# Optimization experiments

Measured on AMD Instinct MI355X. Metric: run time of the kernel, lower is better.

## Reference

```python
import jax, jax.numpy as jnp
import numpy as np

# ---- model constants (match init_kwargs) ----
B, N, T, L = 16384, 32, 300, 1
DIM = 2                      # len(state_index)
DT = 1.0 / (T * L)           # dt = 1/(T*l)
STEPS = T * L                # Euler integration steps (time_steps = STEPS+1)
A_X = 1.0                    # canonical DMP phase constant
TAU = 1.0
HID = 64
OUT = N * DIM + DIM          # fc2_mean output size


def setup_inputs() -> dict:
    key = jax.random.key(0)
    ks = jax.random.split(key, 8)
    s = lambda i, shape, scale: jax.random.normal(ks[i], shape, jnp.float32) * scale
    inp = {
        "state": jax.random.normal(ks[0], (B, 3), jnp.float32),
        "fc1_w": s(1, (HID, 3), 0.3),
        "fc1_b": jnp.full((HID,), 0.1, jnp.float32),
        "fc2m_w": s(2, (OUT, HID), 0.1),
        "fc2m_b": jnp.full((OUT,), 0.1, jnp.float32),
        "sig_w": s(3, (DIM, HID), 0.1),
        "sig_b": jnp.zeros((DIM,), jnp.float32),
        "val_w": s(4, (DIM, HID), 0.1),
        "val_b": jnp.zeros((DIM,), jnp.float32),
    }
    # DMPParameters: gaussian RBF centers on exp-decayed phase, canonical widths
    c = jnp.exp(-A_X * jnp.linspace(0.0, 1.0, N))
    inp["dmp_c"] = c.astype(jnp.float32)
    inp["dmp_sigma2"] = (N ** 1.5 / c / A_X).astype(jnp.float32)
    return inp


def dmp_rollout(w, goal, y0, dy0, a_z, c, sigma2):
    """Euler rollout of DMP transformation system.
    w: [M,N] basis weights, goal/y0/dy0/a_z: [M] per-channel scalars.
    Returns Y, dY, ddY each [M, STEPS+1]."""
    z0 = dy0 * TAU
    b_z = a_z / 4.0

    def step(carry, _):
        x, y, z = carry
        x = x + (-A_X * x) * TAU * DT                       # phase update
        psi = jnp.exp(-0.5 * (x - c) ** 2 / sigma2)          # [N] gaussian RBF
        fx = (w @ psi) * x * (goal - y0) / jnp.sum(psi)      # [M] forcing term
        dz = a_z * (b_z * (goal - y) - z) + fx
        dy = z
        y = y + TAU * dy * DT
        z = z + TAU * dz * DT
        return (x, y, z), (y, dy * TAU, dz * TAU)

    _, (Ys, dYs, ddYs) = jax.lax.scan(
        step, (jnp.float32(1.0), y0, z0), None, length=STEPS)
    Y = jnp.concatenate([y0[None], Ys], axis=0).T            # [M, STEPS+1]
    dY = jnp.concatenate([dy0[None], dYs], axis=0).T
    ddY = jnp.concatenate([z0[None], ddYs], axis=0).T
    return Y, dY, ddY


def reference(state, fc1_w, fc1_b, fc2m_w, fc2m_b, sig_w, sig_b,
              val_w, val_b, dmp_c, dmp_sigma2):
    x = jnp.tanh(state @ fc1_w.T + fc1_b) * 0.1              # [B,64]
    y0 = state[:, :DIM].reshape(-1)                           # [M=B*DIM]
    dy0 = jnp.zeros_like(y0) + 0.01

    # value = fc2_value(x).repeat(1,T).view(-1,T,2).transpose(1,2) == broadcast over T
    v = x @ val_w.T + val_b                                   # [B,2]
    value = jnp.broadcast_to(v[:, :, None], (B, DIM, T))

    sigma = (jax.nn.sigmoid(x @ sig_w.T + sig_b) * 1.0 + 0.001).reshape(-1, DIM, 1)

    ndp_wg = x @ fc2m_w.T + fc2m_b                            # [B, 2N+2]
    goal = ndp_wg[:, :DIM].reshape(-1)                        # [M]
    w = ndp_wg[:, DIM:DIM * (N + 1)].reshape(-1, N)           # [M,N]
    a_z = jnp.clip(ndp_wg[:, -1], 0.5, 30.0)                  # learned a_z (az=True)
    a_z = jnp.broadcast_to(a_z[:, None], (B, DIM)).reshape(-1)

    Y, _, _ = dmp_rollout(w, goal, y0, dy0, a_z, dmp_c, dmp_sigma2)
    y = Y.reshape(B, DIM, -1)[:, :, ::L]                      # [B,2,T+1]
    a = y[:, :, 1:] - y[:, :, :-1]                            # [B,2,T]
    return (a, sigma, value)
```

## Files before the change

### kernel.cpp

```cpp
#include <hip/hip_runtime.h>
#include <hip/hip_bf16.h>

#define NB 32
#define TS 300
#define NBATCH 16384
#define DTF (1.0f/300.0f)
#define A_ELEMS (NBATCH*2*TS)

typedef __attribute__((ext_vector_type(8))) short bf16x8;
typedef __attribute__((ext_vector_type(4))) float f32x4;

static __device__ __forceinline__ ushort f2bf(float f) {
    union { __hip_bfloat16 h; ushort u; } cv;
    cv.h = __float2bfloat16(f);
    return cv.u;
}
static __device__ __forceinline__ float rdlane(float v, int lane) {
    return __int_as_float(__builtin_amdgcn_readlane(__float_as_int(v), lane));
}

__global__ __launch_bounds__(256) void k_fused(
    const float* __restrict__ state,
    const float* __restrict__ fc1_w, const float* __restrict__ fc1_b,
    const float* __restrict__ fc2m_w, const float* __restrict__ fc2m_b,
    const float* __restrict__ sig_w, const float* __restrict__ sig_b,
    const float* __restrict__ val_w, const float* __restrict__ val_b,
    const float* __restrict__ dmp_c, const float* __restrict__ dmp_s2,
    float* __restrict__ sig_out, float* __restrict__ a_out,
    float* __restrict__ v_out)
{
    __shared__ ushort phis[304*NB];
    __shared__ float  wlds[70*64];
    __shared__ float  f1[64*4];
    __shared__ ushort wloc[64*NB];
    __shared__ float4 ppl[64];
    __shared__ float4 xt[4][16][5];

    const int tid = threadIdx.x;
    const int wv  = tid >> 6;
    const int j   = tid & 63;

    for (int i = tid; i < 70*64; i += 256) {
        const int row = i >> 6, col = i & 63;
        float v;
        if (row < 66)      v = fc2m_w[i];
        else if (row < 68) v = sig_w[(row-66)*64 + col];
        else               v = val_w[(row-68)*64 + col];
        const int q = col >> 2, e = col & 3;
        wlds[row*64 + (((q ^ (row & 15)) << 2) | e)] = v;
    }
    if (tid < 64) {
        f1[tid*4+0] = fc1_w[tid*3+0];
        f1[tid*4+1] = fc1_w[tid*3+1];
        f1[tid*4+2] = fc1_w[tid*3+2];
        f1[tid*4+3] = fc1_b[tid];
    }
    {
        const float l2 = log2f(1.0f - DTF);
        for (int t = tid; t < 304; t += 256) {
            ushort row[NB];
            if (t < TS) {
                const float x = exp2f((float)(t + 1) * l2);
                float ps[NB]; float s = 0.0f;
                #pragma unroll
                for (int n = 0; n < NB; ++n) {
                    float d = x - dmp_c[n];
                    float p = __expf(-0.5f * d * d / dmp_s2[n]);
                    ps[n] = p; s += p;
                }
                const float inv = x / s;
                #pragma unroll
                for (int n = 0; n < NB; ++n) row[n] = f2bf(ps[n] * inv);
            } else {
                #pragma unroll
                for (int n = 0; n < NB; ++n) row[n] = 0;
            }
            uint4* dst = (uint4*)(phis + t*NB);
            #pragma unroll
            for (int q4 = 0; q4 < 4; ++q4) {
                union { ushort us[8]; uint4 v; } pk;
                #pragma unroll
                for (int e = 0; e < 8; ++e) pk.us[e] = row[q4*8 + e];
                dst[q4 ^ (t & 3)] = pk.v;
            }
        }
    }
    __syncthreads();

    {
        const int r2 = 64 + (j % 6);
        float wr[64], w2[64];
        #pragma unroll
        for (int q = 0; q < 16; ++q) {
            float4 a  = *(const float4*)(wlds + j*64  + ((q ^ (j  & 15)) << 2));
            wr[q*4+0]=a.x; wr[q*4+1]=a.y; wr[q*4+2]=a.z; wr[q*4+3]=a.w;
            float4 b4 = *(const float4*)(wlds + r2*64 + ((q ^ (r2 & 15)) << 2));
            w2[q*4+0]=b4.x; w2[q*4+1]=b4.y; w2[q*4+2]=b4.z; w2[q*4+3]=b4.w;
        }
        const float bias1 = fc2m_b[j];
        const float bias2 = (r2 < 66) ? fc2m_b[r2] : (r2 < 68) ? sig_b[r2-66] : val_b[r2-68];
        const float4 fw = *(const float4*)(f1 + j*4);

        const int bbase = (blockIdx.x << 5) + (wv << 3);
        float sreg = (j < 24) ? state[bbase*3 + j] : 0.0f;

        for (int it = 0; it < 8; ++it) {
            const float s0  = rdlane(sreg, it*3+0);
            const float s1  = rdlane(sreg, it*3+1);
            const float s2v = rdlane(sreg, it*3+2);
            float pre = fmaf(fw.x, s0, fmaf(fw.y, s1, fmaf(fw.z, s2v, fw.w)));
            float e = __expf(2.0f * pre);
            float h = (1.0f - 2.0f/(e + 1.0f)) * 0.1f;
            float a1 = bias1, a1b = 0.0f, a2 = bias2, a2b = 0.0f;
            #pragma unroll
            for (int k = 0; k < 64; k += 2) {
                const float h0 = rdlane(h, k);
                const float h1 = rdlane(h, k+1);
                a1  = fmaf(wr[k],   h0, a1 );
                a1b = fmaf(wr[k+1], h1, a1b);
                a2  = fmaf(w2[k],   h0, a2 );
                a2b = fmaf(w2[k+1], h1, a2b);
            }
            a1 += a1b; a2 += a2b;
            float az = rdlane(a2, 1);
            az = fminf(fmaxf(az, 0.5f), 30.0f);
            const float vv0 = rdlane(a2, 4);
            const float vv1 = rdlane(a2, 5);
            const int chp = (wv << 4) + (it << 1);
            if (j >= 2) wloc[(chp + ((j-2) >> 5))*NB + ((j-2) & 31)] = f2bf(a1);
            else        wloc[(chp + 1)*NB + 30 + j]                  = f2bf(a2);
            if (j == 2 || j == 3)
                sig_out[(bbase + it)*2 + j - 2] = 1.0f / (1.0f + __expf(-a2)) + 0.001f;
            if (j < 2) {
                const float y0 = (j == 0) ? s0 : s1;
                const float vvl = (j == 0) ? vv0 : vv1;
                ppl[chp + j] = make_float4(a1, a1 - y0, az, vvl);
            }
        }
    }
    __syncthreads();

    const int ch = j & 15;
    const int g  = j >> 4;
    const int chl = (wv << 4) + ch;

    const float4 pp = ppl[chl];
    const float az = pp.z;
    const float Ac = DTF * az * az * 0.25f;
    const float Bc = DTF * az;
    const float Kc = DTF * pp.y;
    const float c0 = Ac * pp.x;
    float y = pp.x - pp.y;
    float z = 0.01f;

    const bf16x8 wb = *(const bf16x8*)(wloc + chl*NB + g*8);
    const ushort* aprow = phis + ch*NB + ((g ^ (ch & 3)) << 3);
    bf16x8 af = *(const bf16x8*)aprow;

    const int mloc = j >> 2;
    const int m_st = (blockIdx.x << 6) + (wv << 4) + mloc;
    const float fv = ppl[(wv << 4) + mloc].w;
    const float4 vsp = make_float4(fv, fv, fv, fv);
    float* aptr = a_out + m_st*TS + (j & 3)*4;
    float* vptr = v_out + m_st*TS + (j & 3)*4;
    const bool tail_ok = (j & 3) < 3;

    const f32x4 zacc = {0.0f, 0.0f, 0.0f, 0.0f};

    for (int c = 0; c < 19; ++c) {
        f32x4 facc = __builtin_amdgcn_mfma_f32_16x16x32_bf16(af, wb, zacc, 0, 0, 0);
        if (c < 18) af = *(const bf16x8*)(aprow + (c + 1)*16*NB);

        float F[16];
        #pragma unroll
        for (int q = 0; q < 4; ++q) {
            float a = facc[q], b = facc[q];
            asm volatile("v_permlane16_swap_b32 %0, %1" : "+v"(a), "+v"(b));
            float a2 = a, b2 = b;
            asm volatile("v_permlane32_swap_b32 %0, %1" : "+v"(a), "+v"(a2));
            asm volatile("v_permlane32_swap_b32 %0, %1" : "+v"(b), "+v"(b2));
            F[0*4+q] = a; F[1*4+q] = b; F[2*4+q] = a2; F[3*4+q] = b2;
        }

        float avq[4] = {0.f, 0.f, 0.f, 0.f};
        #pragma unroll
        for (int i = 0; i < 16; ++i) {
            const float aval = z * DTF;
            if (g == (i >> 2)) avq[i & 3] = aval;
            float u = z + c0;
            u = fmaf(Kc, F[i], u);
            u = fmaf(-Bc, z, u);
            z = fmaf(-Ac, y, u);
            y += aval;
        }

        xt[wv][ch][g] = make_float4(avq[0], avq[1], avq[2], avq[3]);
        if (c < 18 || tail_ok) {
            const float4 s4 = xt[wv][mloc][j & 3];
            *(float4*)aptr = s4;
            *(float4*)vptr = vsp;
        }
        aptr += 16; vptr += 16;
    }
}

extern "C" void kernel_launch(void* const* d_in, const int* in_sizes, int n_in,
                              void* d_out, int out_size, void* d_ws, size_t ws_size,
                              hipStream_t stream) {
    (void)in_sizes; (void)n_in; (void)out_size; (void)d_ws; (void)ws_size;
    const float* state  = (const float*)d_in[0];
    const float* fc1_w  = (const float*)d_in[1];
    const float* fc1_b  = (const float*)d_in[2];
    const float* fc2m_w = (const float*)d_in[3];
    const float* fc2m_b = (const float*)d_in[4];
    const float* sig_w  = (const float*)d_in[5];
    const float* sig_b  = (const float*)d_in[6];
    const float* val_w  = (const float*)d_in[7];
    const float* val_b  = (const float*)d_in[8];
    const float* dmp_c  = (const float*)d_in[9];
    const float* dmp_s2 = (const float*)d_in[10];

    float* out     = (float*)d_out;
    float* a_out   = out;
    float* sig_out = out + A_ELEMS;
    float* v_out   = out + A_ELEMS + NBATCH*2;

    k_fused<<<dim3(512), dim3(256), 0, stream>>>(state, fc1_w, fc1_b, fc2m_w, fc2m_b,
                                                 sig_w, sig_b, val_w, val_b,
                                                 dmp_c, dmp_s2,
                                                 sig_out, a_out, v_out);
}
```

Measured before the change: 33.98 us.

## Compute RBF fragments in registers and stage outputs in LDS for coalesced stores

Drops the shared phase-basis table. Each lane now computes its own bf16 MFMA A-fragments in registers, using cross-lane shuffles to form the normalisation sum. The per-chunk trajectory outputs are staged into a padded LDS tile that reuses the weight-staging memory, then written out as fully contiguous float4 streams after the rollout, and the value broadcast is written up front the same way. A launch-bounds occupancy hint of 2 blocks per CU is added. This trades redundant per-block exp work and higher register pressure (19 held fragments) for removing scattered per-chunk global stores and the phi table.

```diff
diff --git a/kernel.cpp b/kernel.cpp
--- a/kernel.cpp
+++ b/kernel.cpp
@@ -19,7 +19,7 @@
     return __int_as_float(__builtin_amdgcn_readlane(__float_as_int(v), lane));
 }
 
-__global__ __launch_bounds__(256) void k_fused(
+__global__ __launch_bounds__(256, 2) void k_fused(
     const float* __restrict__ state,
     const float* __restrict__ fc1_w, const float* __restrict__ fc1_b,
     const float* __restrict__ fc2m_w, const float* __restrict__ fc2m_b,
@@ -29,16 +29,17 @@
     float* __restrict__ sig_out, float* __restrict__ a_out,
     float* __restrict__ v_out)
 {
-    __shared__ ushort phis[304*NB];
-    __shared__ float  wlds[70*64];
-    __shared__ float  f1[64*4];
-    __shared__ ushort wloc[64*NB];
+    __shared__ float atile[64*308];
     __shared__ float4 ppl[64];
-    __shared__ float4 xt[4][16][5];
+    ushort* wloc = (ushort*)atile;
+    float*  wlds = atile + 1024;
+    float*  f1   = atile + 1024 + 4480;
 
     const int tid = threadIdx.x;
     const int wv  = tid >> 6;
     const int j   = tid & 63;
+    const int ch  = j & 15;
+    const int g   = j >> 4;
 
     for (int i = tid; i < 70*64; i += 256) {
         const int row = i >> 6, col = i & 63;
@@ -55,35 +56,11 @@
         f1[tid*4+2] = fc1_w[tid*3+2];
         f1[tid*4+3] = fc1_b[tid];
     }
-    {
-        const float l2 = log2f(1.0f - DTF);
-        for (int t = tid; t < 304; t += 256) {
-            ushort row[NB];
-            if (t < TS) {
-                const float x = exp2f((float)(t + 1) * l2);
-                float ps[NB]; float s = 0.0f;
-                #pragma unroll
-                for (int n = 0; n < NB; ++n) {
-                    float d = x - dmp_c[n];
-                    float p = __expf(-0.5f * d * d / dmp_s2[n]);
-                    ps[n] = p; s += p;
-                }
-                const float inv = x / s;
-                #pragma unroll
-                for (int n = 0; n < NB; ++n) row[n] = f2bf(ps[n] * inv);
-            } else {
-                #pragma unroll
-                for (int n = 0; n < NB; ++n) row[n] = 0;
-            }
-            uint4* dst = (uint4*)(phis + t*NB);
-            #pragma unroll
-            for (int q4 = 0; q4 < 4; ++q4) {
-                union { ushort us[8]; uint4 v; } pk;
-                #pragma unroll
-                for (int e = 0; e < 8; ++e) pk.us[e] = row[q4*8 + e];
-                dst[q4 ^ (t & 3)] = pk.v;
-            }
-        }
+    float cn[8], rs2[8];
+    #pragma unroll
+    for (int e = 0; e < 8; ++e) {
+        cn[e]  = dmp_c[g*8 + e];
+        rs2[e] = -0.5f / dmp_s2[g*8 + e];
     }
     __syncthreads();
 
@@ -140,10 +117,21 @@
     }
     __syncthreads();
 
-    const int ch = j & 15;
-    const int g  = j >> 4;
+    const int blk = blockIdx.x;
+    const float* pplf = (const float*)ppl;
+
+    #pragma unroll 1
+    for (int it = 0; it < 19; ++it) {
+        const int i = it*256 + tid;
+        if (i < 4800) {
+            const int chv = (int)((unsigned)i / 75u);
+            const float vv = pplf[chv*4 + 3];
+            *(float4*)(v_out + blk*19200 + i*4) = make_float4(vv, vv, vv, vv);
+        }
+    }
+
     const int chl = (wv << 4) + ch;
-
+    const bf16x8 wb = *(const bf16x8*)(wloc + chl*NB + g*8);
     const float4 pp = ppl[chl];
     const float az = pp.z;
     const float Ac = DTF * az * az * 0.25f;
@@ -153,23 +141,36 @@
     float y = pp.x - pp.y;
     float z = 0.01f;
 
-    const bf16x8 wb = *(const bf16x8*)(wloc + chl*NB + g*8);
-    const ushort* aprow = phis + ch*NB + ((g ^ (ch & 3)) << 3);
-    bf16x8 af = *(const bf16x8*)aprow;
-
-    const int mloc = j >> 2;
-    const int m_st = (blockIdx.x << 6) + (wv << 4) + mloc;
-    const float fv = ppl[(wv << 4) + mloc].w;
-    const float4 vsp = make_float4(fv, fv, fv, fv);
-    float* aptr = a_out + m_st*TS + (j & 3)*4;
-    float* vptr = v_out + m_st*TS + (j & 3)*4;
-    const bool tail_ok = (j & 3) < 3;
+    bf16x8 af[19];
+    {
+        const float l2 = log2f(1.0f - DTF);
+        #pragma unroll
+        for (int c = 0; c < 19; ++c) {
+            const int t = c*16 + ch;
+            const float x = exp2f((float)(t + 1) * l2);
+            float p[8]; float s = 0.0f;
+            #pragma unroll
+            for (int e = 0; e < 8; ++e) {
+                const float d = x - cn[e];
+                p[e] = __expf(d * d * rs2[e]);
+                s += p[e];
+            }
+            s += __shfl_xor(s, 16, 64);
+            s += __shfl_xor(s, 32, 64);
+            const float inv = (t < TS) ? x / s : 0.0f;
+            union { bf16x8 v; ushort u[8]; } pk;
+            #pragma unroll
+            for (int e = 0; e < 8; ++e) pk.u[e] = f2bf(p[e] * inv);
+            af[c] = pk.v;
+        }
+    }
+    __syncthreads();
 
     const f32x4 zacc = {0.0f, 0.0f, 0.0f, 0.0f};
-
+    float* arow = atile + chl*308;
+    #pragma unroll
     for (int c = 0; c < 19; ++c) {
-        f32x4 facc = __builtin_amdgcn_mfma_f32_16x16x32_bf16(af, wb, zacc, 0, 0, 0);
-        if (c < 18) af = *(const bf16x8*)(aprow + (c + 1)*16*NB);
+        f32x4 facc = __builtin_amdgcn_mfma_f32_16x16x32_bf16(af[c], wb, zacc, 0, 0, 0);
 
         float F[16];
         #pragma unroll
@@ -182,7 +183,7 @@
             F[0*4+q] = a; F[1*4+q] = b; F[2*4+q] = a2; F[3*4+q] = b2;
         }
 
-        float avq[4] = {0.f, 0.f, 0.f, 0.f};
+        float avq[4];
         #pragma unroll
         for (int i = 0; i < 16; ++i) {
             const float aval = z * DTF;
@@ -193,14 +194,19 @@
             z = fmaf(-Ac, y, u);
             y += aval;
         }
-
-        xt[wv][ch][g] = make_float4(avq[0], avq[1], avq[2], avq[3]);
-        if (c < 18 || tail_ok) {
-            const float4 s4 = xt[wv][mloc][j & 3];
-            *(float4*)aptr = s4;
-            *(float4*)vptr = vsp;
-        }
-        aptr += 16; vptr += 16;
+        *(float4*)(arow + (c*4 + g)*4) = make_float4(avq[0], avq[1], avq[2], avq[3]);
+    }
+    __syncthreads();
+
+    #pragma unroll 1
+    for (int it = 0; it < 19; ++it) {
+        const int i = it*256 + tid;
+        if (i < 4800) {
+            const int chv = (int)((unsigned)i / 75u);
+            const int l   = i - chv*75;
+            const float4 val = *(const float4*)(atile + chv*308 + l*4);
+            *(float4*)(a_out + blk*19200 + i*4) = val;
+        }
     }
 }
 
```

Measured after the change: 42.74 us. 25.7% more time.

## Split DMP rollout: MFMA forcing to LDS, one lane per channel scan

Applied to the files above, without the earlier changes.

All waves first compute the forcing terms with MFMA and store them as bf16 in a shared LDS buffer that reuses the weight staging area. Wave 0 then runs the Euler recurrence with one lane per channel, streaming 4 steps at a time and writing float4 outputs directly. This replaces the per-chunk permlane shuffles and the 16-step serial chain run by every lane. The other three waves write the broadcast value output in parallel, and occupancy is requested at 2 blocks per CU. The recurrence is now done by only one wave per block, so more serial latency sits on a single wave. Storing the forcing term in bf16 adds extra rounding.

```diff
diff --git a/kernel.cpp b/kernel.cpp
--- a/kernel.cpp
+++ b/kernel.cpp
@@ -19,7 +19,7 @@
     return __int_as_float(__builtin_amdgcn_readlane(__float_as_int(v), lane));
 }
 
-__global__ __launch_bounds__(256) void k_fused(
+__global__ __launch_bounds__(256, 2) void k_fused(
     const float* __restrict__ state,
     const float* __restrict__ fc1_w, const float* __restrict__ fc1_b,
     const float* __restrict__ fc2m_w, const float* __restrict__ fc2m_b,
@@ -29,12 +29,14 @@
     float* __restrict__ sig_out, float* __restrict__ a_out,
     float* __restrict__ v_out)
 {
-    __shared__ ushort phis[304*NB];
-    __shared__ float  wlds[70*64];
-    __shared__ float  f1[64*4];
-    __shared__ ushort wloc[64*NB];
-    __shared__ float4 ppl[64];
-    __shared__ float4 xt[4][16][5];
+    __shared__ float smemf[16128];
+    char* smem = (char*)smemf;
+    ushort* phis = (ushort*)smem;
+    ushort* wloc = (ushort*)(smem + 19456);
+    float*  pplf = (float*)(smem + 23552);
+    char*   ftb  = smem + 24576;
+    float*  wlds = (float*)(smem + 24576);
+    float*  f1   = (float*)(smem + 42496);
 
     const int tid = threadIdx.x;
     const int wv  = tid >> 6;
@@ -134,73 +136,84 @@
             if (j < 2) {
                 const float y0 = (j == 0) ? s0 : s1;
                 const float vvl = (j == 0) ? vv0 : vv1;
-                ppl[chp + j] = make_float4(a1, a1 - y0, az, vvl);
+                *(float4*)(pplf + (chp + j)*4) = make_float4(a1, a1 - y0, az, vvl);
             }
         }
     }
     __syncthreads();
 
-    const int ch = j & 15;
-    const int g  = j >> 4;
-    const int chl = (wv << 4) + ch;
-
-    const float4 pp = ppl[chl];
-    const float az = pp.z;
-    const float Ac = DTF * az * az * 0.25f;
-    const float Bc = DTF * az;
-    const float Kc = DTF * pp.y;
-    const float c0 = Ac * pp.x;
-    float y = pp.x - pp.y;
-    float z = 0.01f;
-
-    const bf16x8 wb = *(const bf16x8*)(wloc + chl*NB + g*8);
-    const ushort* aprow = phis + ch*NB + ((g ^ (ch & 3)) << 3);
-    bf16x8 af = *(const bf16x8*)aprow;
-
-    const int mloc = j >> 2;
-    const int m_st = (blockIdx.x << 6) + (wv << 4) + mloc;
-    const float fv = ppl[(wv << 4) + mloc].w;
-    const float4 vsp = make_float4(fv, fv, fv, fv);
-    float* aptr = a_out + m_st*TS + (j & 3)*4;
-    float* vptr = v_out + m_st*TS + (j & 3)*4;
-    const bool tail_ok = (j & 3) < 3;
-
-    const f32x4 zacc = {0.0f, 0.0f, 0.0f, 0.0f};
-
-    for (int c = 0; c < 19; ++c) {
-        f32x4 facc = __builtin_amdgcn_mfma_f32_16x16x32_bf16(af, wb, zacc, 0, 0, 0);
-        if (c < 18) af = *(const bf16x8*)(aprow + (c + 1)*16*NB);
-
-        float F[16];
-        #pragma unroll
-        for (int q = 0; q < 4; ++q) {
-            float a = facc[q], b = facc[q];
-            asm volatile("v_permlane16_swap_b32 %0, %1" : "+v"(a), "+v"(b));
-            float a2 = a, b2 = b;
-            asm volatile("v_permlane32_swap_b32 %0, %1" : "+v"(a), "+v"(a2));
-            asm volatile("v_permlane32_swap_b32 %0, %1" : "+v"(b), "+v"(b2));
-            F[0*4+q] = a; F[1*4+q] = b; F[2*4+q] = a2; F[3*4+q] = b2;
-        }
-
-        float avq[4] = {0.f, 0.f, 0.f, 0.f};
-        #pragma unroll
-        for (int i = 0; i < 16; ++i) {
-            const float aval = z * DTF;
-            if (g == (i >> 2)) avq[i & 3] = aval;
-            float u = z + c0;
-            u = fmaf(Kc, F[i], u);
-            u = fmaf(-Bc, z, u);
-            z = fmaf(-Ac, y, u);
-            y += aval;
-        }
-
-        xt[wv][ch][g] = make_float4(avq[0], avq[1], avq[2], avq[3]);
-        if (c < 18 || tail_ok) {
-            const float4 s4 = xt[wv][mloc][j & 3];
-            *(float4*)aptr = s4;
-            *(float4*)vptr = vsp;
-        }
-        aptr += 16; vptr += 16;
+    {
+        const int ch = j & 15, g = j >> 4;
+        const int chl = (wv << 4) + ch;
+        const bf16x8 wb = *(const bf16x8*)(wloc + chl*NB + g*8);
+        const ushort* aprow = phis + ch*NB + ((g ^ (ch & 3)) << 3);
+        bf16x8 af = *(const bf16x8*)aprow;
+        const f32x4 zacc = {0.0f, 0.0f, 0.0f, 0.0f};
+        char* wp = ftb + chl*624 + g*8;
+        for (int c = 0; c < 19; ++c) {
+            f32x4 facc = __builtin_amdgcn_mfma_f32_16x16x32_bf16(af, wb, zacc, 0, 0, 0);
+            if (c < 18) af = *(const bf16x8*)(aprow + (c + 1)*16*NB);
+            const uint w0 = (uint)f2bf(facc[0]) | ((uint)f2bf(facc[1]) << 16);
+            const uint w1 = (uint)f2bf(facc[2]) | ((uint)f2bf(facc[3]) << 16);
+            *(uint2*)(wp + c*32) = make_uint2(w0, w1);
+        }
+    }
+    __syncthreads();
+
+    if (wv == 0) {
+        const float4 pp = *(const float4*)(pplf + j*4);
+        const float az = pp.z;
+        const float Ac = DTF * az * az * 0.25f;
+        const float Bc = DTF * az;
+        const float Kc = DTF * pp.y;
+        const float c0 = Ac * pp.x;
+        const float OmB = 1.0f - Bc;
+        float y = pp.x - pp.y;
+        float z = 0.01f;
+
+        const char* fp = ftb + j*624;
+        float* aptr = a_out + ((blockIdx.x << 6) + j)*TS;
+
+        uint2 fc = *(const uint2*)fp;
+        #pragma unroll 1
+        for (int s = 0; s < 75; ++s) {
+            const uint2 fn = *(const uint2*)(fp + s*8 + 8);
+            const float F0 = __uint_as_float(fc.x << 16);
+            const float F1 = __uint_as_float(fc.x & 0xffff0000u);
+            const float F2 = __uint_as_float(fc.y << 16);
+            const float F3 = __uint_as_float(fc.y & 0xffff0000u);
+            float a0, a1, a2, a3;
+            {
+                a0 = z * DTF;
+                const float t2 = fmaf(-Ac, y, fmaf(Kc, F0, c0));
+                y += a0;  z = fmaf(OmB, z, t2);
+            }
+            {
+                a1 = z * DTF;
+                const float t2 = fmaf(-Ac, y, fmaf(Kc, F1, c0));
+                y += a1;  z = fmaf(OmB, z, t2);
+            }
+            {
+                a2 = z * DTF;
+                const float t2 = fmaf(-Ac, y, fmaf(Kc, F2, c0));
+                y += a2;  z = fmaf(OmB, z, t2);
+            }
+            {
+                a3 = z * DTF;
+                const float t2 = fmaf(-Ac, y, fmaf(Kc, F3, c0));
+                y += a3;  z = fmaf(OmB, z, t2);
+            }
+            *(float4*)(aptr + s*4) = make_float4(a0, a1, a2, a3);
+            fc = fn;
+        }
+    } else {
+        float* vbase = v_out + blockIdx.x * 19200;
+        #pragma unroll 1
+        for (int i = tid - 64; i < 4800; i += 192) {
+            const int chv = (int)((unsigned)i / 75u);
+            const float vv = pplf[chv*4 + 3];
+            *(float4*)(vbase + i*4) = make_float4(vv, vv, vv, vv);
+        }
     }
 }
 
```

After: 42.04 us. +23.7%, slower.

## Split fused kernel into prep, MFMA head, and rollout kernels via workspace

Applied to the files above, without the earlier changes.

Replaces the single fused kernel with three launches. A one-block prep kernel builds the bf16 RBF phase table and the MFMA-ready bf16 weight fragments once. A head kernel computes the MLP with MFMA instead of per-lane readlane FMAs. The rollout reads the precomputed table and parameters from global workspace instead of rebuilding them in every block, and folds the Euler update into fewer FMAs. This removes redundant per-block setup and serial readlane work, at the cost of two extra launches, serialization through a single-block kernel, and round-trips through global memory.

```diff
diff --git a/kernel.cpp b/kernel.cpp
--- a/kernel.cpp
+++ b/kernel.cpp
@@ -15,161 +15,208 @@
     cv.h = __float2bfloat16(f);
     return cv.u;
 }
-static __device__ __forceinline__ float rdlane(float v, int lane) {
-    return __int_as_float(__builtin_amdgcn_readlane(__float_as_int(v), lane));
-}
-
-__global__ __launch_bounds__(256) void k_fused(
-    const float* __restrict__ state,
-    const float* __restrict__ fc1_w, const float* __restrict__ fc1_b,
+
+
+__global__ __launch_bounds__(1024) void k_prep(
     const float* __restrict__ fc2m_w, const float* __restrict__ fc2m_b,
     const float* __restrict__ sig_w, const float* __restrict__ sig_b,
     const float* __restrict__ val_w, const float* __restrict__ val_b,
     const float* __restrict__ dmp_c, const float* __restrict__ dmp_s2,
-    float* __restrict__ sig_out, float* __restrict__ a_out,
-    float* __restrict__ v_out)
+    uint4* __restrict__ wsPhi, uint4* __restrict__ wsB,
+    float* __restrict__ wsBias)
 {
-    __shared__ ushort phis[304*NB];
-    __shared__ float  wlds[70*64];
-    __shared__ float  f1[64*4];
-    __shared__ ushort wloc[64*NB];
-    __shared__ float4 ppl[64];
-    __shared__ float4 xt[4][16][5];
+    const int t = threadIdx.x;
+    if (t < 304) {
+        ushort row[NB];
+        if (t < TS) {
+            const float x = exp2f((float)(t + 1) * log2f(1.0f - DTF));
+            float ps[NB]; float s = 0.0f;
+            #pragma unroll
+            for (int n = 0; n < NB; ++n) {
+                float d = x - dmp_c[n];
+                float p = __expf(-0.5f * d * d / dmp_s2[n]);
+                ps[n] = p; s += p;
+            }
+            const float inv = x / s;
+            #pragma unroll
+            for (int n = 0; n < NB; ++n) row[n] = f2bf(ps[n] * inv);
+        } else {
+            #pragma unroll
+            for (int n = 0; n < NB; ++n) row[n] = 0;
+        }
+        #pragma unroll
+        for (int g0 = 0; g0 < 4; ++g0) {
+            union { ushort us[8]; uint4 v; } pk;
+            #pragma unroll
+            for (int e = 0; e < 8; ++e) pk.us[e] = row[g0*8 + e];
+            wsPhi[(t >> 4)*64 + g0*16 + (t & 15)] = pk.v;
+        }
+    } else if (t < 944) {
+        const int e = t - 304;
+        const int T = e >> 7, kk = (e >> 6) & 1, lane = e & 63;
+        const int r = T*16 + (lane & 15);
+        const int k0 = kk*32 + (lane >> 4)*8;
+        union { ushort us[8]; uint4 v; } pk;
+        if (r < 70) {
+            const float* src = (r < 66) ? (fc2m_w + r*64 + k0)
+                             : (r < 68) ? (sig_w + (r-66)*64 + k0)
+                             : (val_w + (r-68)*64 + k0);
+            #pragma unroll
+            for (int i = 0; i < 8; ++i) pk.us[i] = f2bf(src[i]);
+        } else {
+            #pragma unroll
+            for (int i = 0; i < 8; ++i) pk.us[i] = 0;
+        }
+        wsB[e] = pk.v;
+    } else {
+        const int r = t - 944;
+        wsBias[r] = (r < 66) ? fc2m_b[r] : (r < 68) ? sig_b[r-66]
+                  : (r < 70) ? val_b[r-68] : 0.0f;
+    }
+}
+
+__global__ __launch_bounds__(256) void k_head(
+    const float* __restrict__ state,
+    const float* __restrict__ fc1_w, const float* __restrict__ fc1_b,
+    const uint4* __restrict__ wsB, const float* __restrict__ wsBias,
+    float* __restrict__ sig_out, float* __restrict__ pbuf,
+    ushort* __restrict__ wbuf16)
+{
+    __shared__ float f1[64*4];
+    __shared__ float biasl[80];
+    __shared__ float hlds[4*16*68];
+    __shared__ float ct[4*16*84];
 
     const int tid = threadIdx.x;
     const int wv  = tid >> 6;
-    const int j   = tid & 63;
-
-    for (int i = tid; i < 70*64; i += 256) {
-        const int row = i >> 6, col = i & 63;
-        float v;
-        if (row < 66)      v = fc2m_w[i];
-        else if (row < 68) v = sig_w[(row-66)*64 + col];
-        else               v = val_w[(row-68)*64 + col];
-        const int q = col >> 2, e = col & 3;
-        wlds[row*64 + (((q ^ (row & 15)) << 2) | e)] = v;
-    }
+    const int l   = tid & 63;
+    const int b16 = l & 15;
+    const int g   = l >> 4;
+
     if (tid < 64) {
         f1[tid*4+0] = fc1_w[tid*3+0];
         f1[tid*4+1] = fc1_w[tid*3+1];
         f1[tid*4+2] = fc1_w[tid*3+2];
         f1[tid*4+3] = fc1_b[tid];
     }
+    if (tid < 80) biasl[tid] = wsBias[tid];
+    __syncthreads();
+
+    const int bbase = blockIdx.x*64 + wv*16;
+    const int bglob = bbase + b16;
+    const float s0 = state[bglob*3+0], s1 = state[bglob*3+1], s2 = state[bglob*3+2];
+
+    float* hrow = hlds + wv*1088 + b16*68;
+    #pragma unroll
+    for (int i = 0; i < 16; ++i) {
+        const int hid = g + 4*i;
+        const float4 fw = *(const float4*)(f1 + hid*4);
+        const float pre = fmaf(fw.x, s0, fmaf(fw.y, s1, fmaf(fw.z, s2, fw.w)));
+        const float e = __expf(2.0f * pre);
+        hrow[hid] = (1.0f - 2.0f/(e + 1.0f)) * 0.1f;
+    }
+
+    bf16x8 A0, A1;
     {
-        const float l2 = log2f(1.0f - DTF);
-        for (int t = tid; t < 304; t += 256) {
-            ushort row[NB];
-            if (t < TS) {
-                const float x = exp2f((float)(t + 1) * l2);
-                float ps[NB]; float s = 0.0f;
-                #pragma unroll
-                for (int n = 0; n < NB; ++n) {
-                    float d = x - dmp_c[n];
-                    float p = __expf(-0.5f * d * d / dmp_s2[n]);
-                    ps[n] = p; s += p;
-                }
-                const float inv = x / s;
-                #pragma unroll
-                for (int n = 0; n < NB; ++n) row[n] = f2bf(ps[n] * inv);
-            } else {
-                #pragma unroll
-                for (int n = 0; n < NB; ++n) row[n] = 0;
-            }
-            uint4* dst = (uint4*)(phis + t*NB);
-            #pragma unroll
-            for (int q4 = 0; q4 < 4; ++q4) {
-                union { ushort us[8]; uint4 v; } pk;
-                #pragma unroll
-                for (int e = 0; e < 8; ++e) pk.us[e] = row[q4*8 + e];
-                dst[q4 ^ (t & 3)] = pk.v;
-            }
-        }
-    }
-    __syncthreads();
-
-    {
-        const int r2 = 64 + (j % 6);
-        float wr[64], w2[64];
-        #pragma unroll
-        for (int q = 0; q < 16; ++q) {
-            float4 a  = *(const float4*)(wlds + j*64  + ((q ^ (j  & 15)) << 2));
-            wr[q*4+0]=a.x; wr[q*4+1]=a.y; wr[q*4+2]=a.z; wr[q*4+3]=a.w;
-            float4 b4 = *(const float4*)(wlds + r2*64 + ((q ^ (r2 & 15)) << 2));
-            w2[q*4+0]=b4.x; w2[q*4+1]=b4.y; w2[q*4+2]=b4.z; w2[q*4+3]=b4.w;
-        }
-        const float bias1 = fc2m_b[j];
-        const float bias2 = (r2 < 66) ? fc2m_b[r2] : (r2 < 68) ? sig_b[r2-66] : val_b[r2-68];
-        const float4 fw = *(const float4*)(f1 + j*4);
-
-        const int bbase = (blockIdx.x << 5) + (wv << 3);
-        float sreg = (j < 24) ? state[bbase*3 + j] : 0.0f;
-
-        for (int it = 0; it < 8; ++it) {
-            const float s0  = rdlane(sreg, it*3+0);
-            const float s1  = rdlane(sreg, it*3+1);
-            const float s2v = rdlane(sreg, it*3+2);
-            float pre = fmaf(fw.x, s0, fmaf(fw.y, s1, fmaf(fw.z, s2v, fw.w)));
-            float e = __expf(2.0f * pre);
-            float h = (1.0f - 2.0f/(e + 1.0f)) * 0.1f;
-            float a1 = bias1, a1b = 0.0f, a2 = bias2, a2b = 0.0f;
-            #pragma unroll
-            for (int k = 0; k < 64; k += 2) {
-                const float h0 = rdlane(h, k);
-                const float h1 = rdlane(h, k+1);
-                a1  = fmaf(wr[k],   h0, a1 );
-                a1b = fmaf(wr[k+1], h1, a1b);
-                a2  = fmaf(w2[k],   h0, a2 );
-                a2b = fmaf(w2[k+1], h1, a2b);
-            }
-            a1 += a1b; a2 += a2b;
-            float az = rdlane(a2, 1);
-            az = fminf(fmaxf(az, 0.5f), 30.0f);
-            const float vv0 = rdlane(a2, 4);
-            const float vv1 = rdlane(a2, 5);
-            const int chp = (wv << 4) + (it << 1);
-            if (j >= 2) wloc[(chp + ((j-2) >> 5))*NB + ((j-2) & 31)] = f2bf(a1);
-            else        wloc[(chp + 1)*NB + 30 + j]                  = f2bf(a2);
-            if (j == 2 || j == 3)
-                sig_out[(bbase + it)*2 + j - 2] = 1.0f / (1.0f + __expf(-a2)) + 0.001f;
-            if (j < 2) {
-                const float y0 = (j == 0) ? s0 : s1;
-                const float vvl = (j == 0) ? vv0 : vv1;
-                ppl[chp + j] = make_float4(a1, a1 - y0, az, vvl);
-            }
-        }
-    }
-    __syncthreads();
-
+        const float* hr = hlds + wv*1088 + b16*68 + g*8;
+        const float4 h0 = *(const float4*)(hr),     h1 = *(const float4*)(hr + 4);
+        const float4 h2 = *(const float4*)(hr + 32), h3 = *(const float4*)(hr + 36);
+        union { bf16x8 v; ushort u[8]; } p0, p1;
+        p0.u[0]=f2bf(h0.x); p0.u[1]=f2bf(h0.y); p0.u[2]=f2bf(h0.z); p0.u[3]=f2bf(h0.w);
+        p0.u[4]=f2bf(h1.x); p0.u[5]=f2bf(h1.y); p0.u[6]=f2bf(h1.z); p0.u[7]=f2bf(h1.w);
+        p1.u[0]=f2bf(h2.x); p1.u[1]=f2bf(h2.y); p1.u[2]=f2bf(h2.z); p1.u[3]=f2bf(h2.w);
+        p1.u[4]=f2bf(h3.x); p1.u[5]=f2bf(h3.y); p1.u[6]=f2bf(h3.z); p1.u[7]=f2bf(h3.w);
+        A0 = p0.v; A1 = p1.v;
+    }
+
+    float* ctw = ct + wv*1344;
+    const f32x4 zacc = {0.0f, 0.0f, 0.0f, 0.0f};
+    #pragma unroll
+    for (int T = 0; T < 5; ++T) {
+        union { uint4 q; bf16x8 v; } B0, B1;
+        B0.q = wsB[(T*2+0)*64 + l];
+        B1.q = wsB[(T*2+1)*64 + l];
+        f32x4 acc = __builtin_amdgcn_mfma_f32_16x16x32_bf16(A0, B0.v, zacc, 0, 0, 0);
+        acc = __builtin_amdgcn_mfma_f32_16x16x32_bf16(A1, B1.v, acc, 0, 0, 0);
+        const int r = T*16 + b16;
+        const float bs = biasl[r];
+        #pragma unroll
+        for (int reg = 0; reg < 4; ++reg)
+            ctw[(g*4 + reg)*84 + r] = acc[reg] + bs;
+    }
+
+    uint* wout = (uint*)wbuf16;
+    #pragma unroll 1
+    for (int b = 0; b < 16; ++b) {
+        if (l < 32) {
+            const float2 wp = *(const float2*)(ctw + b*84 + 2 + 2*l);
+            wout[(bbase + b)*32 + l] = (uint)f2bf(wp.x) | ((uint)f2bf(wp.y) << 16);
+        }
+    }
+    if (l < 16) {
+        const float* cb = ctw + l*84;
+        const float goal = cb[0];
+        const float az = fminf(fmaxf(cb[65], 0.5f), 30.0f);
+        const float y0 = state[(bbase + l)*3 + 0];
+        *(float4*)(pbuf + ((bbase + l)*2 + 0)*4) = make_float4(goal, goal - y0, az, cb[68]);
+    } else if (l < 32) {
+        const int b = l - 16;
+        const float* cb = ctw + b*84;
+        const float goal = cb[1];
+        const float az = fminf(fmaxf(cb[65], 0.5f), 30.0f);
+        const float y0 = state[(bbase + b)*3 + 1];
+        *(float4*)(pbuf + ((bbase + b)*2 + 1)*4) = make_float4(goal, goal - y0, az, cb[69]);
+    } else if (l < 48) {
+        const int b = l - 32;
+        const float* cb = ctw + b*84;
+        const float sg0 = 1.0f / (1.0f + __expf(-cb[66])) + 0.001f;
+        const float sg1 = 1.0f / (1.0f + __expf(-cb[67])) + 0.001f;
+        *(float2*)(sig_out + (bbase + b)*2) = make_float2(sg0, sg1);
+    }
+}
+
+__global__ __launch_bounds__(256) void k_roll(
+    const uint4* __restrict__ wsPhi, const float* __restrict__ pbuf,
+    const ushort* __restrict__ wbuf16, float* __restrict__ a_out,
+    float* __restrict__ v_out)
+{
+    __shared__ float4 xt[4][16][5];
+    const int tid = threadIdx.x;
+    const int wv = tid >> 6;
+    const int j  = tid & 63;
     const int ch = j & 15;
     const int g  = j >> 4;
-    const int chl = (wv << 4) + ch;
-
-    const float4 pp = ppl[chl];
+    const int m  = (blockIdx.x << 6) + (wv << 4) + ch;
+
+    const float4 pp = *(const float4*)(pbuf + m*4);
     const float az = pp.z;
     const float Ac = DTF * az * az * 0.25f;
-    const float Bc = DTF * az;
     const float Kc = DTF * pp.y;
     const float c0 = Ac * pp.x;
+    const float OmB = 1.0f - DTF * az;
     float y = pp.x - pp.y;
     float z = 0.01f;
 
-    const bf16x8 wb = *(const bf16x8*)(wloc + chl*NB + g*8);
-    const ushort* aprow = phis + ch*NB + ((g ^ (ch & 3)) << 3);
-    bf16x8 af = *(const bf16x8*)aprow;
+    const bf16x8 wb = *(const bf16x8*)(wbuf16 + m*NB + g*8);
+    const bf16x8* ap = (const bf16x8*)wsPhi;
+    bf16x8 af = ap[j];
 
     const int mloc = j >> 2;
     const int m_st = (blockIdx.x << 6) + (wv << 4) + mloc;
-    const float fv = ppl[(wv << 4) + mloc].w;
-    const float4 vsp = make_float4(fv, fv, fv, fv);
     float* aptr = a_out + m_st*TS + (j & 3)*4;
     float* vptr = v_out + m_st*TS + (j & 3)*4;
     const bool tail_ok = (j & 3) < 3;
+    float4 vsp;
+    {
+        const float fv = pbuf[((blockIdx.x << 6) + (wv << 4) + mloc)*4 + 3];
+        vsp = make_float4(fv, fv, fv, fv);
+    }
 
     const f32x4 zacc = {0.0f, 0.0f, 0.0f, 0.0f};
 
     for (int c = 0; c < 19; ++c) {
         f32x4 facc = __builtin_amdgcn_mfma_f32_16x16x32_bf16(af, wb, zacc, 0, 0, 0);
-        if (c < 18) af = *(const bf16x8*)(aprow + (c + 1)*16*NB);
+        if (c < 18) af = ap[(c + 1)*64 + j];
 
         float F[16];
         #pragma unroll
@@ -187,10 +234,9 @@
         for (int i = 0; i < 16; ++i) {
             const float aval = z * DTF;
             if (g == (i >> 2)) avq[i & 3] = aval;
-            float u = z + c0;
-            u = fmaf(Kc, F[i], u);
-            u = fmaf(-Bc, z, u);
-            z = fmaf(-Ac, y, u);
+            float t2 = fmaf(Kc, F[i], c0);
+            t2 = fmaf(-Ac, y, t2);
+            z = fmaf(OmB, z, t2);
             y += aval;
         }
 
@@ -207,7 +253,7 @@
 extern "C" void kernel_launch(void* const* d_in, const int* in_sizes, int n_in,
                               void* d_out, int out_size, void* d_ws, size_t ws_size,
                               hipStream_t stream) {
-    (void)in_sizes; (void)n_in; (void)out_size; (void)d_ws; (void)ws_size;
+    (void)in_sizes; (void)n_in; (void)out_size; (void)ws_size;
     const float* state  = (const float*)d_in[0];
     const float* fc1_w  = (const float*)d_in[1];
     const float* fc1_b  = (const float*)d_in[2];
@@ -225,8 +271,17 @@
     float* sig_out = out + A_ELEMS;
     float* v_out   = out + A_ELEMS + NBATCH*2;
 
-    k_fused<<<dim3(512), dim3(256), 0, stream>>>(state, fc1_w, fc1_b, fc2m_w, fc2m_b,
-                                                 sig_w, sig_b, val_w, val_b,
-                                                 dmp_c, dmp_s2,
-                                                 sig_out, a_out, v_out);
-}
+    char* ws = (char*)d_ws;
+    uint4*  wsPhi  = (uint4*)ws;
+    uint4*  wsB    = (uint4*)(ws + 19456);
+    float*  wsBias = (float*)(ws + 29696);
+    float*  pbuf   = (float*)(ws + 32768);
+    ushort* wbuf16 = (ushort*)(ws + 557056);
+
+    k_prep<<<dim3(1), dim3(1024), 0, stream>>>(fc2m_w, fc2m_b, sig_w, sig_b,
+                                               val_w, val_b, dmp_c, dmp_s2,
+                                               wsPhi, wsB, wsBias);
+    k_head<<<dim3(256), dim3(256), 0, stream>>>(state, fc1_w, fc1_b, wsB, wsBias,
+                                                sig_out, pbuf, wbuf16);
+    k_roll<<<dim3(512), dim3(256), 0, stream>>>(wsPhi, pbuf, wbuf16, a_out, v_out);
+}
```

Result: faster. 33.31 us (-2.0%).
